# Kernel tuning notes

Measured on AMD Instinct MI355X. Metric: run time of the kernel, lower is better.

Reference implementation:

```python
import jax, jax.numpy as jnp
import numpy as np

B, F, D, V = 8192, 26, 32, 100000
H1, H2 = 128, 128  # cin_size
U1, U2 = 400, 400  # dnn hidden units


def setup_inputs() -> dict:
    key = jax.random.key(0)
    ks = jax.random.split(key, 12)
    s = 0.05  # keep activations/sigmoid in a sane range
    return {
        "dense_inputs": jax.random.normal(ks[0], (B, 13), jnp.float32),
        "sparse_inputs": jax.random.randint(ks[1], (B, F), 0, V, jnp.int32),
        "E": jax.random.normal(ks[2], (F, V, D), jnp.float32) * s,
        "W_cin0": jax.random.normal(ks[3], (F, F, H1), jnp.float32) * s,
        "W_cin1": jax.random.normal(ks[4], (F, H1, H2), jnp.float32) * s,
        "W1": jax.random.normal(ks[5], (F * D, U1), jnp.float32) * s,
        "b1": jnp.zeros((U1,), jnp.float32),
        "W2": jax.random.normal(ks[6], (U1, U2), jnp.float32) * s,
        "b2": jnp.zeros((U2,), jnp.float32),
        "w_lin": jax.random.normal(ks[7], (F, 1), jnp.float32) * s,
        "b_lin": jnp.zeros((1,), jnp.float32),
        "w_out": jax.random.normal(ks[8], (1 + H1 + H2 + U2 + 13, 1), jnp.float32) * s,
        "b_out": jnp.zeros((1,), jnp.float32),
    }


def reference(dense_inputs, sparse_inputs, E, W_cin0, W_cin1, W1, b1, W2, b2,
              w_lin, b_lin, w_out, b_out):
    # Linear part: Dense(1) applied to raw (cast) sparse ids, as in the TF code.
    linear_out = sparse_inputs.astype(jnp.float32) @ w_lin + b_lin  # [B,1]

    # Embedding lookup: per-field tables. embed[b,f,:] = E[f, sparse[b,f], :]
    embed = E[jnp.arange(F)[None, :], sparse_inputs]  # [B,F,D]

    # CIN. The split->matmul->reshape->conv1d chain is exactly:
    #   x_{k+1}[b,h,d] = sum_{i,j} W_k[i,j,h] * X0[b,i,d] * x_k[b,j,d]
    X0 = embed
    x1 = jnp.einsum('bid,bjd,ijh->bhd', X0, X0, W_cin0)   # [B,H1,D]
    x2 = jnp.einsum('bid,bjd,ijh->bhd', X0, x1, W_cin1)   # [B,H2,D]
    cin_out = jnp.concatenate([x1, x2], axis=1).sum(axis=-1)  # [B,H1+H2]

    # DNN on flattened embeddings (dropout rate 0 -> identity at inference).
    v = embed.reshape(B, F * D)
    h = jax.nn.relu(v @ W1 + b1)
    h = jax.nn.relu(h @ W2 + b2)  # [B,U2]

    total = jnp.concatenate([linear_out, cin_out, h, dense_inputs], axis=-1)
    return jax.nn.sigmoid(total @ w_out + b_out)  # [B,1]
```

## Files before the change

### kernel.cpp

```cpp
#include <hip/hip_runtime.h>
#include <hip/hip_bf16.h>
#include <math.h>

typedef __attribute__((ext_vector_type(8))) short bf16x8;
typedef __attribute__((ext_vector_type(4))) float f32x4;

#define B_ 8192
#define F_ 26
#define D_ 32
#define V_ 100000

static const size_t OFF_VB   = 0;
static const size_t OFF_FD0  = 13631488;
static const size_t OFF_H1B  = 13664256;
static const size_t OFF_W1T  = 20217856;
static const size_t OFF_W2T  = 20883456;
static const size_t OFF_K2T  = 21203456;

static __device__ __forceinline__ unsigned short f2b(float f) {
    unsigned int u = __float_as_uint(f);
    return (unsigned short)((u + 0x7FFF + ((u >> 16) & 1)) >> 16);
}
static __device__ __forceinline__ unsigned short f2bt(float f) {
    return (unsigned short)(__float_as_uint(f) >> 16);
}
static __device__ __forceinline__ unsigned int pk2t(float a, float b) {
    return __builtin_amdgcn_perm(__float_as_uint(b), __float_as_uint(a), 0x07060302u);
}
static __device__ __forceinline__ float bf2f(unsigned short u) {
    return __uint_as_float(((unsigned int)u) << 16);
}

static __device__ __forceinline__ void transpose_body(
    const float* __restrict__ src, unsigned short* __restrict__ dst,
    int K, int N, int bx, int by)
{
    __shared__ float tl[32][33];
    const int lx = threadIdx.x & 31, ly = threadIdx.x >> 5;
    const int n0 = bx * 32, k0 = by * 32;
#pragma unroll
    for (int i = 0; i < 4; ++i) {
        int k = k0 + ly + i * 8, n = n0 + lx;
        if (k < K && n < N) tl[ly + i * 8][lx] = src[(size_t)k * N + n];
    }
    __syncthreads();
#pragma unroll
    for (int i = 0; i < 4; ++i) {
        int n = n0 + ly + i * 8, k = k0 + lx;
        if (k < K && n < N) dst[(size_t)n * K + k] = f2b(tl[lx][ly + i * 8]);
    }
}

__global__ __launch_bounds__(256) void k0_all(
    const float* __restrict__ W1, const float* __restrict__ W2,
    const float* __restrict__ W0, const float* __restrict__ Wc1,
    const float* __restrict__ wout,
    unsigned short* __restrict__ W1t, unsigned short* __restrict__ W2t,
    unsigned short* __restrict__ K2T)
{
    __shared__ float Mi[128];
    int bid = blockIdx.x;
    const int t = threadIdx.x;
    if (bid < 338) { transpose_body(W1, W1t, 832, 400, bid % 13, bid / 13); return; }
    bid -= 338;
    if (bid < 169) { transpose_body(W2, W2t, 400, 400, bid % 13, bid / 13); return; }
    bid -= 169;
    const int i = bid;
    if (t < 128) {
        float m = 0.f;
        if (i < F_) {
            const float* row = Wc1 + ((size_t)i * 128 + t) * 128;
            for (int h = 0; h < 128; h += 4) {
                float4 a = *(const float4*)(row + h);
                m = fmaf(a.x, wout[129 + h],     m);
                m = fmaf(a.y, wout[129 + h + 1], m);
                m = fmaf(a.z, wout[129 + h + 2], m);
                m = fmaf(a.w, wout[129 + h + 3], m);
            }
        } else if (i == F_) {
            m = wout[1 + t];
        }
        Mi[t] = m;
    }
    __syncthreads();
    for (int q = t; q < 352; q += 256) {
        float s = 0.f;
        if (q < 351 && i <= F_) {
            int a = 0, base = 0;
            while (base + (F_ - a) <= q) { base += F_ - a; ++a; }
            int b = a + (q - base);
            const float* r0 = W0 + ((size_t)a * F_ + b) * 128;
            const float* r1 = W0 + ((size_t)b * F_ + a) * 128;
            if (a == b) {
                for (int j = 0; j < 128; j += 4) {
                    float4 w = *(const float4*)(r0 + j);
                    s += w.x * Mi[j] + w.y * Mi[j + 1] + w.z * Mi[j + 2] + w.w * Mi[j + 3];
                }
            } else {
                for (int j = 0; j < 128; j += 4) {
                    float4 w  = *(const float4*)(r0 + j);
                    float4 w1 = *(const float4*)(r1 + j);
                    s += (w.x + w1.x) * Mi[j]     + (w.y + w1.y) * Mi[j + 1]
                       + (w.z + w1.z) * Mi[j + 2] + (w.w + w1.w) * Mi[j + 3];
                }
            }
        }
        unsigned short hi = f2b(s);
        float lo = s - bf2f(hi);
        K2T[q * 32 + i] = hi;
        K2T[11264 + q * 32 + i] = f2b(lo);
    }
}

__global__ __launch_bounds__(256) void k1_embed_cin(
    const int*   __restrict__ sparse,
    const float* __restrict__ E,
    const unsigned short* __restrict__ K2T,
    const float* __restrict__ wlin,
    const float* __restrict__ blin,
    const float* __restrict__ wout,
    unsigned short* __restrict__ vb,
    float* __restrict__ fdot0)
{
    __shared__ __align__(16) unsigned short embT[32][40];
    __shared__ unsigned int PQ[352];
    __shared__ int idxs[F_];
    __shared__ float red[4];

    const int b = blockIdx.x, t = threadIdx.x;
    float cind = 0.f;

    if (t < F_) {
        int id = sparse[b * F_ + t];
        idxs[t] = id;
        cind = (float)id * wlin[t] * wout[0];
        int base = F_ * t - (t * (t - 1)) / 2;
        for (int j = t; j < F_; ++j)
            PQ[base + j - t] = (unsigned)t | ((unsigned)j << 16);
    }
    if (t == F_) PQ[351] = 0u;
    if (t >= 32 && t < 64) {
        int d = t - 32;
        embT[d][26] = 0x3F80;
        embT[d][27] = 0; embT[d][28] = 0; embT[d][29] = 0;
        embT[d][30] = 0; embT[d][31] = 0;
    }
    __syncthreads();

    if (t < 208) {
        int f = t >> 3, q = t & 7;
        float4 v4 = *(const float4*)(E + ((size_t)f * V_ + idxs[f]) * D_ + q * 4);
        uint2 uu; uu.x = pk2t(v4.x, v4.y); uu.y = pk2t(v4.z, v4.w);
        *(uint2*)(vb + (size_t)b * 832 + f * 32 + q * 4) = uu;
        embT[q * 4 + 0][f] = f2bt(v4.x);
        embT[q * 4 + 1][f] = f2bt(v4.y);
        embT[q * 4 + 2][f] = f2bt(v4.z);
        embT[q * 4 + 3][f] = f2bt(v4.w);
    }
    __syncthreads();

    const int wave = t >> 6, lane = t & 63;
    const int lr = lane & 15, lg = lane >> 4;
    const int mt = wave & 1;
    const int nb = wave >> 1;
    bf16x8 af = *(const bf16x8*)&embT[mt * 16 + lr][lg * 8];
    const unsigned short* ebase = &embT[mt * 16 + lg * 4][0];
    const unsigned short* Kb = K2T + (size_t)lr * 32 + lg * 8;

#pragma unroll
    for (int s = 0; s < 11; ++s) {
        const int nt = 2 * s + nb;
        bf16x8 bh = *(const bf16x8*)(Kb + (size_t)nt * 512);
        bf16x8 bl = *(const bf16x8*)(Kb + 11264 + (size_t)nt * 512);
        f32x4 h = {};
        h = __builtin_amdgcn_mfma_f32_16x16x32_bf16(af, bl, h, 0, 0, 0);
        h = __builtin_amdgcn_mfma_f32_16x16x32_bf16(af, bh, h, 0, 0, 0);
        unsigned pq = PQ[nt * 16 + lr];
        int oi = (int)(pq & 0xFFFFu), oj = (int)(pq >> 16);
#pragma unroll
        for (int r = 0; r < 4; ++r) {
            float ei = bf2f(ebase[r * 40 + oi]);
            float ej = bf2f(ebase[r * 40 + oj]);
            cind = fmaf(ei * ej, h[r], cind);
        }
    }

#pragma unroll
    for (int off = 1; off <= 32; off <<= 1) cind += __shfl_xor(cind, off, 64);
    if (lane == 0) red[wave] = cind;
    __syncthreads();
    if (t == 0) fdot0[b] = red[0] + red[1] + red[2] + red[3] + blin[0] * wout[0];
}

static __device__ __forceinline__ void gemm_core(
    const unsigned short* __restrict__ A, int lda,
    const unsigned short* __restrict__ Bt, int ldb, int N,
    int m0, int n0, int kbase, int kend,
    unsigned short (*As)[40], unsigned short (*Bs)[40],
    f32x4 (*acc)[2])
{
    const int t = threadIdx.x;
    const int wave = t >> 6, lane = t & 63;
    const int lr = lane & 15, lg = lane >> 4;
    const int wn = wave * 32;
    const int ar = t >> 2, kg = (t & 3) * 8;

    const unsigned short* aptr = A  + (size_t)(m0 + ar) * lda + kbase + kg;
    const unsigned short* bp0  = Bt + (size_t)(n0 + ar) * ldb + kbase + kg;
    const unsigned short* bp1  = Bt + (size_t)(n0 + 64 + ar) * ldb + kbase + kg;
    const bool bn0 = (n0 + ar) < N, bn1 = (n0 + 64 + ar) < N;
    const uint4 z4 = make_uint4(0u, 0u, 0u, 0u);
    const int nkt = (kend - kbase + 31) >> 5;
    uint4 av, bv0, bv1;
    {
        int k = kbase + kg;
        av  = (k < kend)        ? *(const uint4*)aptr : z4;
        bv0 = (bn0 && k < kend) ? *(const uint4*)bp0  : z4;
        bv1 = (bn1 && k < kend) ? *(const uint4*)bp1  : z4;
    }
    for (int kt = 0; kt < nkt; ++kt) {
        *(uint4*)&As[ar][kg]      = av;
        *(uint4*)&Bs[ar][kg]      = bv0;
        *(uint4*)&Bs[64 + ar][kg] = bv1;
        __syncthreads();
        if (kt + 1 < nkt) {
            int kn = kbase + (kt + 1) * 32 + kg;
            av  = (kn < kend)        ? *(const uint4*)(aptr + (kt + 1) * 32) : z4;
            bv0 = (bn0 && kn < kend) ? *(const uint4*)(bp0  + (kt + 1) * 32) : z4;
            bv1 = (bn1 && kn < kend) ? *(const uint4*)(bp1  + (kt + 1) * 32) : z4;
        }
        bf16x8 af[4], bfr[2];
#pragma unroll
        for (int i = 0; i < 4; ++i) af[i]  = *(const bf16x8*)&As[i * 16 + lr][lg * 8];
#pragma unroll
        for (int j = 0; j < 2; ++j) bfr[j] = *(const bf16x8*)&Bs[wn + j * 16 + lr][lg * 8];
#pragma unroll
        for (int i = 0; i < 4; ++i)
#pragma unroll
            for (int j = 0; j < 2; ++j)
                acc[i][j] = __builtin_amdgcn_mfma_f32_16x16x32_bf16(af[i], bfr[j], acc[i][j], 0, 0, 0);
        __syncthreads();
    }
}

__global__ __launch_bounds__(256) void k2_h1(
    const unsigned short* __restrict__ vb, const unsigned short* __restrict__ W1t,
    const float* __restrict__ b1, unsigned short* __restrict__ h1b)
{
    __shared__ __align__(16) unsigned short As[64][40];
    __shared__ __align__(16) unsigned short Bs[128][40];
    const int t = threadIdx.x;
    const int wave = t >> 6, lane = t & 63;
    const int lr = lane & 15, lg = lane >> 4;
    const int m0 = blockIdx.y * 64, n0 = blockIdx.x * 128;
    f32x4 acc[4][2] = {};
    gemm_core(vb, 832, W1t, 832, 400, m0, n0, 0, 832, As, Bs, acc);
#pragma unroll
    for (int i = 0; i < 4; ++i) {
        int mrow = m0 + i * 16 + lg * 4;
#pragma unroll
        for (int j = 0; j < 2; ++j) {
            int col = n0 + wave * 32 + j * 16 + lr;
            if (col >= 400) continue;
            float bb = b1[col];
#pragma unroll
            for (int r = 0; r < 4; ++r)
                h1b[(size_t)(mrow + r) * 400 + col] = f2bt(fmaxf(acc[i][j][r] + bb, 0.f));
        }
    }
}

__global__ __launch_bounds__(256) void k2_h2f(
    const unsigned short* __restrict__ h1b, const unsigned short* __restrict__ W2t,
    const float* __restrict__ b2, const float* __restrict__ wout,
    const float* __restrict__ fdot0, const float* __restrict__ dense,
    const float* __restrict__ bout, float* __restrict__ out)
{
    __shared__ __align__(16) unsigned short As[32][424];
    __shared__ float red[4][32];
    const int t = threadIdx.x;
    const int m0 = blockIdx.x * 32;

    for (int idx = t; idx < 1600; idx += 256) {
        int row = idx / 50, c = idx - row * 50;
        *(uint4*)&As[row][c * 8] = *(const uint4*)(h1b + (size_t)(m0 + row) * 400 + c * 8);
    }
    if (t < 96) {
        int row = t / 3, c = t - row * 3;
        uint4 z = make_uint4(0u, 0u, 0u, 0u);
        *(uint4*)&As[row][400 + c * 8] = z;
    }
    __syncthreads();

    const int wave = t >> 6, lane = t & 63;
    const int lr = lane & 15, lg = lane >> 4;
    float s[2][4] = {};

    for (int nt = wave; nt < 25; nt += 4) {
        f32x4 acc0 = {}, acc1 = {};
        const unsigned short* bp = W2t + (size_t)(nt * 16 + lr) * 400 + lg * 8;
#pragma unroll
        for (int kt = 0; kt < 13; ++kt) {
            const int kk = kt * 32 + lg * 8;
            bf16x8 bw = {};
            if (kk < 400) bw = *(const bf16x8*)(bp + kt * 32);
            bf16x8 a0 = *(const bf16x8*)&As[lr][kk];
            bf16x8 a1 = *(const bf16x8*)&As[16 + lr][kk];
            acc0 = __builtin_amdgcn_mfma_f32_16x16x32_bf16(a0, bw, acc0, 0, 0, 0);
            acc1 = __builtin_amdgcn_mfma_f32_16x16x32_bf16(a1, bw, acc1, 0, 0, 0);
        }
        const int col = nt * 16 + lr;
        const float bb = b2[col], wo = wout[257 + col];
#pragma unroll
        for (int r = 0; r < 4; ++r) {
            s[0][r] = fmaf(fmaxf(acc0[r] + bb, 0.f), wo, s[0][r]);
            s[1][r] = fmaf(fmaxf(acc1[r] + bb, 0.f), wo, s[1][r]);
        }
    }
#pragma unroll
    for (int mt = 0; mt < 2; ++mt)
#pragma unroll
        for (int r = 0; r < 4; ++r) {
            float v = s[mt][r];
            v += __shfl_xor(v, 1, 64);
            v += __shfl_xor(v, 2, 64);
            v += __shfl_xor(v, 4, 64);
            v += __shfl_xor(v, 8, 64);
            if (lr == 0) red[wave][mt * 16 + lg * 4 + r] = v;
        }
    __syncthreads();
    if (t < 32) {
        const int b = m0 + t;
        float tot = red[0][t] + red[1][t] + red[2][t] + red[3][t]
                  + fdot0[b] + bout[0];
#pragma unroll
        for (int q = 0; q < 13; ++q)
            tot = fmaf(dense[(size_t)b * 13 + q], wout[657 + q], tot);
        out[b] = 1.f / (1.f + expf(-tot));
    }
}

extern "C" void kernel_launch(void* const* d_in, const int* in_sizes, int n_in,
                              void* d_out, int out_size, void* d_ws, size_t ws_size,
                              hipStream_t stream) {
    const float* dense  = (const float*)d_in[0];
    const int*   sparse = (const int*)  d_in[1];
    const float* E      = (const float*)d_in[2];
    const float* W0     = (const float*)d_in[3];
    const float* Wc1    = (const float*)d_in[4];
    const float* W1     = (const float*)d_in[5];
    const float* b1     = (const float*)d_in[6];
    const float* W2     = (const float*)d_in[7];
    const float* b2     = (const float*)d_in[8];
    const float* wlin   = (const float*)d_in[9];
    const float* blin   = (const float*)d_in[10];
    const float* wout   = (const float*)d_in[11];
    const float* bout   = (const float*)d_in[12];
    float* out = (float*)d_out;

    char* ws = (char*)d_ws;
    unsigned short* vb    = (unsigned short*)(ws + OFF_VB);
    float*          fdot0 = (float*)(ws + OFF_FD0);
    unsigned short* h1b   = (unsigned short*)(ws + OFF_H1B);
    unsigned short* W1t   = (unsigned short*)(ws + OFF_W1T);
    unsigned short* W2t   = (unsigned short*)(ws + OFF_W2T);
    unsigned short* K2T   = (unsigned short*)(ws + OFF_K2T);

    k0_all<<<338 + 169 + 32, 256, 0, stream>>>(W1, W2, W0, Wc1, wout, W1t, W2t, K2T);
    k1_embed_cin<<<B_, 256, 0, stream>>>(sparse, E, K2T, wlin, blin, wout, vb, fdot0);
    k2_h1<<<dim3(4, 128), 256, 0, stream>>>(vb, W1t, b1, h1b);
    k2_h2f<<<256, 256, 0, stream>>>(h1b, W2t, b2, wout, fdot0, dense, bout, out);
}
```

Measured before the change: 510.9 us.

## Fuse both DNN layers into one kernel keeping hidden activations in LDS

Merges the first-layer GEMM and the second-layer GEMM plus output epilogue into a single 512-thread kernel. Each block holds a 32-row tile of embeddings and keeps the first hidden layer in shared memory, so the h1 round trip through global memory and one launch go away. Weight matrices are transposed and zero-padded to 512 columns so the inner loops need no bounds checks. The trade-off is only 256 blocks for the first GEMM, compared with 512 before, and each block streams the full W1 and W2 from L2 without sharing them through LDS. That lowers parallelism and raises L2 traffic for the weights.

```diff
diff --git a/kernel.cpp b/kernel.cpp
--- a/kernel.cpp
+++ b/kernel.cpp
@@ -12,10 +12,11 @@
 
 static const size_t OFF_VB   = 0;
 static const size_t OFF_FD0  = 13631488;
-static const size_t OFF_H1B  = 13664256;
-static const size_t OFF_W1T  = 20217856;
-static const size_t OFF_W2T  = 20883456;
-static const size_t OFF_K2T  = 21203456;
+static const size_t OFF_W1T  = 13664256;
+static const size_t OFF_W2T  = 14516224;
+static const size_t OFF_K2T  = 15040512;
+static const size_t OFF_B2P  = 15085568;
+static const size_t OFF_WO2P = 15087616;
 
 static __device__ __forceinline__ unsigned short f2b(float f) {
     unsigned int u = __float_as_uint(f);
@@ -31,9 +32,9 @@
     return __uint_as_float(((unsigned int)u) << 16);
 }
 
-static __device__ __forceinline__ void transpose_body(
+static __device__ __forceinline__ void transpose_pad(
     const float* __restrict__ src, unsigned short* __restrict__ dst,
-    int K, int N, int bx, int by)
+    int K, int N, int Kpad, int Npad, int bx, int by)
 {
     __shared__ float tl[32][33];
     const int lx = threadIdx.x & 31, ly = threadIdx.x >> 5;
@@ -41,74 +42,82 @@
 #pragma unroll
     for (int i = 0; i < 4; ++i) {
         int k = k0 + ly + i * 8, n = n0 + lx;
-        if (k < K && n < N) tl[ly + i * 8][lx] = src[(size_t)k * N + n];
+        tl[ly + i * 8][lx] = (k < K && n < N) ? src[(size_t)k * N + n] : 0.f;
     }
     __syncthreads();
 #pragma unroll
     for (int i = 0; i < 4; ++i) {
         int n = n0 + ly + i * 8, k = k0 + lx;
-        if (k < K && n < N) dst[(size_t)n * K + k] = f2b(tl[lx][ly + i * 8]);
+        if (n < Npad && k < Kpad) dst[(size_t)n * Kpad + k] = f2b(tl[lx][ly + i * 8]);
     }
 }
 
 __global__ __launch_bounds__(256) void k0_all(
     const float* __restrict__ W1, const float* __restrict__ W2,
     const float* __restrict__ W0, const float* __restrict__ Wc1,
-    const float* __restrict__ wout,
+    const float* __restrict__ wout, const float* __restrict__ b2,
     unsigned short* __restrict__ W1t, unsigned short* __restrict__ W2t,
-    unsigned short* __restrict__ K2T)
+    unsigned short* __restrict__ K2T,
+    float* __restrict__ b2p, float* __restrict__ wo2p)
 {
     __shared__ float Mi[128];
     int bid = blockIdx.x;
     const int t = threadIdx.x;
-    if (bid < 338) { transpose_body(W1, W1t, 832, 400, bid % 13, bid / 13); return; }
-    bid -= 338;
-    if (bid < 169) { transpose_body(W2, W2t, 400, 400, bid % 13, bid / 13); return; }
-    bid -= 169;
-    const int i = bid;
-    if (t < 128) {
-        float m = 0.f;
-        if (i < F_) {
-            const float* row = Wc1 + ((size_t)i * 128 + t) * 128;
-            for (int h = 0; h < 128; h += 4) {
-                float4 a = *(const float4*)(row + h);
-                m = fmaf(a.x, wout[129 + h],     m);
-                m = fmaf(a.y, wout[129 + h + 1], m);
-                m = fmaf(a.z, wout[129 + h + 2], m);
-                m = fmaf(a.w, wout[129 + h + 3], m);
-            }
-        } else if (i == F_) {
-            m = wout[1 + t];
-        }
-        Mi[t] = m;
-    }
-    __syncthreads();
-    for (int q = t; q < 352; q += 256) {
-        float s = 0.f;
-        if (q < 351 && i <= F_) {
-            int a = 0, base = 0;
-            while (base + (F_ - a) <= q) { base += F_ - a; ++a; }
-            int b = a + (q - base);
-            const float* r0 = W0 + ((size_t)a * F_ + b) * 128;
-            const float* r1 = W0 + ((size_t)b * F_ + a) * 128;
-            if (a == b) {
-                for (int j = 0; j < 128; j += 4) {
-                    float4 w = *(const float4*)(r0 + j);
-                    s += w.x * Mi[j] + w.y * Mi[j + 1] + w.z * Mi[j + 2] + w.w * Mi[j + 3];
+    if (bid < 416) { transpose_pad(W1, W1t, 832, 400, 832, 512, bid % 16, bid / 16); return; }
+    bid -= 416;
+    if (bid < 256) { transpose_pad(W2, W2t, 400, 400, 512, 512, bid % 16, bid / 16); return; }
+    bid -= 256;
+    if (bid < 32) {
+        const int i = bid;
+        if (t < 128) {
+            float m = 0.f;
+            if (i < F_) {
+                const float* row = Wc1 + ((size_t)i * 128 + t) * 128;
+                for (int h = 0; h < 128; h += 4) {
+                    float4 a = *(const float4*)(row + h);
+                    m = fmaf(a.x, wout[129 + h],     m);
+                    m = fmaf(a.y, wout[129 + h + 1], m);
+                    m = fmaf(a.z, wout[129 + h + 2], m);
+                    m = fmaf(a.w, wout[129 + h + 3], m);
                 }
-            } else {
-                for (int j = 0; j < 128; j += 4) {
-                    float4 w  = *(const float4*)(r0 + j);
-                    float4 w1 = *(const float4*)(r1 + j);
-                    s += (w.x + w1.x) * Mi[j]     + (w.y + w1.y) * Mi[j + 1]
-                       + (w.z + w1.z) * Mi[j + 2] + (w.w + w1.w) * Mi[j + 3];
+            } else if (i == F_) {
+                m = wout[1 + t];
+            }
+            Mi[t] = m;
+        }
+        __syncthreads();
+        for (int q = t; q < 352; q += 256) {
+            float s = 0.f;
+            if (q < 351 && i <= F_) {
+                int a = 0, base = 0;
+                while (base + (F_ - a) <= q) { base += F_ - a; ++a; }
+                int b = a + (q - base);
+                const float* r0 = W0 + ((size_t)a * F_ + b) * 128;
+                const float* r1 = W0 + ((size_t)b * F_ + a) * 128;
+                if (a == b) {
+                    for (int j = 0; j < 128; j += 4) {
+                        float4 w = *(const float4*)(r0 + j);
+                        s += w.x * Mi[j] + w.y * Mi[j + 1] + w.z * Mi[j + 2] + w.w * Mi[j + 3];
+                    }
+                } else {
+                    for (int j = 0; j < 128; j += 4) {
+                        float4 w  = *(const float4*)(r0 + j);
+                        float4 w1 = *(const float4*)(r1 + j);
+                        s += (w.x + w1.x) * Mi[j]     + (w.y + w1.y) * Mi[j + 1]
+                           + (w.z + w1.z) * Mi[j + 2] + (w.w + w1.w) * Mi[j + 3];
+                    }
                 }
             }
-        }
-        unsigned short hi = f2b(s);
-        float lo = s - bf2f(hi);
-        K2T[q * 32 + i] = hi;
-        K2T[11264 + q * 32 + i] = f2b(lo);
+            unsigned short hi = f2b(s);
+            float lo = s - bf2f(hi);
+            K2T[q * 32 + i] = hi;
+            K2T[11264 + q * 32 + i] = f2b(lo);
+        }
+        return;
+    }
+    for (int c = t; c < 512; c += 256) {
+        b2p[c]  = (c < 400) ? b2[c] : 0.f;
+        wo2p[c] = (c < 400) ? wout[257 + c] : 0.f;
     }
 }
 
@@ -192,147 +201,135 @@
     if (t == 0) fdot0[b] = red[0] + red[1] + red[2] + red[3] + blin[0] * wout[0];
 }
 
-static __device__ __forceinline__ void gemm_core(
-    const unsigned short* __restrict__ A, int lda,
-    const unsigned short* __restrict__ Bt, int ldb, int N,
-    int m0, int n0, int kbase, int kend,
-    unsigned short (*As)[40], unsigned short (*Bs)[40],
-    f32x4 (*acc)[2])
+__global__ __launch_bounds__(512) void k23_mlp(
+    const unsigned short* __restrict__ vb,
+    const unsigned short* __restrict__ W1t,
+    const unsigned short* __restrict__ W2t,
+    const float* __restrict__ b1,
+    const float* __restrict__ b2p,
+    const float* __restrict__ wo2p,
+    const float* __restrict__ fdot0,
+    const float* __restrict__ dense,
+    const float* __restrict__ wout,
+    const float* __restrict__ bout,
+    float* __restrict__ out)
 {
+    __shared__ __align__(16) unsigned short As1[32][840];
+    __shared__ __align__(16) unsigned short h1s[32][520];
+    __shared__ float red[8][32];
+
     const int t = threadIdx.x;
+    const int m0 = blockIdx.x * 32;
+
+    {
+        const int row = t >> 4, c0 = t & 15;
+        const unsigned short* src = vb + (size_t)(m0 + row) * 832;
+#pragma unroll
+        for (int j = 0; j < 7; ++j) {
+            int c = c0 + j * 16;
+            if (c < 104) *(uint4*)&As1[row][c * 8] = *(const uint4*)(src + c * 8);
+        }
+    }
+    __syncthreads();
+
     const int wave = t >> 6, lane = t & 63;
     const int lr = lane & 15, lg = lane >> 4;
-    const int wn = wave * 32;
-    const int ar = t >> 2, kg = (t & 3) * 8;
-
-    const unsigned short* aptr = A  + (size_t)(m0 + ar) * lda + kbase + kg;
-    const unsigned short* bp0  = Bt + (size_t)(n0 + ar) * ldb + kbase + kg;
-    const unsigned short* bp1  = Bt + (size_t)(n0 + 64 + ar) * ldb + kbase + kg;
-    const bool bn0 = (n0 + ar) < N, bn1 = (n0 + 64 + ar) < N;
-    const uint4 z4 = make_uint4(0u, 0u, 0u, 0u);
-    const int nkt = (kend - kbase + 31) >> 5;
-    uint4 av, bv0, bv1;
+
     {
-        int k = kbase + kg;
-        av  = (k < kend)        ? *(const uint4*)aptr : z4;
-        bv0 = (bn0 && k < kend) ? *(const uint4*)bp0  : z4;
-        bv1 = (bn1 && k < kend) ? *(const uint4*)bp1  : z4;
-    }
-    for (int kt = 0; kt < nkt; ++kt) {
-        *(uint4*)&As[ar][kg]      = av;
-        *(uint4*)&Bs[ar][kg]      = bv0;
-        *(uint4*)&Bs[64 + ar][kg] = bv1;
-        __syncthreads();
-        if (kt + 1 < nkt) {
-            int kn = kbase + (kt + 1) * 32 + kg;
-            av  = (kn < kend)        ? *(const uint4*)(aptr + (kt + 1) * 32) : z4;
-            bv0 = (bn0 && kn < kend) ? *(const uint4*)(bp0  + (kt + 1) * 32) : z4;
-            bv1 = (bn1 && kn < kend) ? *(const uint4*)(bp1  + (kt + 1) * 32) : z4;
-        }
-        bf16x8 af[4], bfr[2];
-#pragma unroll
-        for (int i = 0; i < 4; ++i) af[i]  = *(const bf16x8*)&As[i * 16 + lr][lg * 8];
-#pragma unroll
-        for (int j = 0; j < 2; ++j) bfr[j] = *(const bf16x8*)&Bs[wn + j * 16 + lr][lg * 8];
-#pragma unroll
-        for (int i = 0; i < 4; ++i)
-#pragma unroll
-            for (int j = 0; j < 2; ++j)
-                acc[i][j] = __builtin_amdgcn_mfma_f32_16x16x32_bf16(af[i], bfr[j], acc[i][j], 0, 0, 0);
-        __syncthreads();
-    }
-}
-
-__global__ __launch_bounds__(256) void k2_h1(
-    const unsigned short* __restrict__ vb, const unsigned short* __restrict__ W1t,
-    const float* __restrict__ b1, unsigned short* __restrict__ h1b)
-{
-    __shared__ __align__(16) unsigned short As[64][40];
-    __shared__ __align__(16) unsigned short Bs[128][40];
-    const int t = threadIdx.x;
-    const int wave = t >> 6, lane = t & 63;
-    const int lr = lane & 15, lg = lane >> 4;
-    const int m0 = blockIdx.y * 64, n0 = blockIdx.x * 128;
-    f32x4 acc[4][2] = {};
-    gemm_core(vb, 832, W1t, 832, 400, m0, n0, 0, 832, As, Bs, acc);
-#pragma unroll
-    for (int i = 0; i < 4; ++i) {
-        int mrow = m0 + i * 16 + lg * 4;
-#pragma unroll
-        for (int j = 0; j < 2; ++j) {
-            int col = n0 + wave * 32 + j * 16 + lr;
-            if (col >= 400) continue;
-            float bb = b1[col];
-#pragma unroll
-            for (int r = 0; r < 4; ++r)
-                h1b[(size_t)(mrow + r) * 400 + col] = f2bt(fmaxf(acc[i][j][r] + bb, 0.f));
-        }
-    }
-}
-
-__global__ __launch_bounds__(256) void k2_h2f(
-    const unsigned short* __restrict__ h1b, const unsigned short* __restrict__ W2t,
-    const float* __restrict__ b2, const float* __restrict__ wout,
-    const float* __restrict__ fdot0, const float* __restrict__ dense,
-    const float* __restrict__ bout, float* __restrict__ out)
-{
-    __shared__ __align__(16) unsigned short As[32][424];
-    __shared__ float red[4][32];
-    const int t = threadIdx.x;
-    const int m0 = blockIdx.x * 32;
-
-    for (int idx = t; idx < 1600; idx += 256) {
-        int row = idx / 50, c = idx - row * 50;
-        *(uint4*)&As[row][c * 8] = *(const uint4*)(h1b + (size_t)(m0 + row) * 400 + c * 8);
-    }
-    if (t < 96) {
-        int row = t / 3, c = t - row * 3;
-        uint4 z = make_uint4(0u, 0u, 0u, 0u);
-        *(uint4*)&As[row][400 + c * 8] = z;
-    }
-    __syncthreads();
-
-    const int wave = t >> 6, lane = t & 63;
-    const int lr = lane & 15, lg = lane >> 4;
-    float s[2][4] = {};
-
-    for (int nt = wave; nt < 25; nt += 4) {
-        f32x4 acc0 = {}, acc1 = {};
-        const unsigned short* bp = W2t + (size_t)(nt * 16 + lr) * 400 + lg * 8;
-#pragma unroll
-        for (int kt = 0; kt < 13; ++kt) {
+        f32x4 acc[4][2] = {};
+        const unsigned short* bp0 = W1t + (size_t)((wave +  0) * 16 + lr) * 832 + lg * 8;
+        const unsigned short* bp1 = W1t + (size_t)((wave +  8) * 16 + lr) * 832 + lg * 8;
+        const unsigned short* bp2 = W1t + (size_t)((wave + 16) * 16 + lr) * 832 + lg * 8;
+        const unsigned short* bp3 = W1t + (size_t)((wave + 24) * 16 + lr) * 832 + lg * 8;
+#pragma unroll 2
+        for (int kt = 0; kt < 26; ++kt) {
             const int kk = kt * 32 + lg * 8;
-            bf16x8 bw = {};
-            if (kk < 400) bw = *(const bf16x8*)(bp + kt * 32);
-            bf16x8 a0 = *(const bf16x8*)&As[lr][kk];
-            bf16x8 a1 = *(const bf16x8*)&As[16 + lr][kk];
-            acc0 = __builtin_amdgcn_mfma_f32_16x16x32_bf16(a0, bw, acc0, 0, 0, 0);
-            acc1 = __builtin_amdgcn_mfma_f32_16x16x32_bf16(a1, bw, acc1, 0, 0, 0);
-        }
-        const int col = nt * 16 + lr;
-        const float bb = b2[col], wo = wout[257 + col];
+            bf16x8 a0 = *(const bf16x8*)&As1[lr][kk];
+            bf16x8 a1 = *(const bf16x8*)&As1[16 + lr][kk];
+            bf16x8 b0 = *(const bf16x8*)(bp0 + kt * 32);
+            bf16x8 b1w = *(const bf16x8*)(bp1 + kt * 32);
+            bf16x8 b2w = *(const bf16x8*)(bp2 + kt * 32);
+            bf16x8 b3w = *(const bf16x8*)(bp3 + kt * 32);
+            acc[0][0] = __builtin_amdgcn_mfma_f32_16x16x32_bf16(a0, b0,  acc[0][0], 0, 0, 0);
+            acc[0][1] = __builtin_amdgcn_mfma_f32_16x16x32_bf16(a1, b0,  acc[0][1], 0, 0, 0);
+            acc[1][0] = __builtin_amdgcn_mfma_f32_16x16x32_bf16(a0, b1w, acc[1][0], 0, 0, 0);
+            acc[1][1] = __builtin_amdgcn_mfma_f32_16x16x32_bf16(a1, b1w, acc[1][1], 0, 0, 0);
+            acc[2][0] = __builtin_amdgcn_mfma_f32_16x16x32_bf16(a0, b2w, acc[2][0], 0, 0, 0);
+            acc[2][1] = __builtin_amdgcn_mfma_f32_16x16x32_bf16(a1, b2w, acc[2][1], 0, 0, 0);
+            acc[3][0] = __builtin_amdgcn_mfma_f32_16x16x32_bf16(a0, b3w, acc[3][0], 0, 0, 0);
+            acc[3][1] = __builtin_amdgcn_mfma_f32_16x16x32_bf16(a1, b3w, acc[3][1], 0, 0, 0);
+        }
+#pragma unroll
+        for (int q = 0; q < 4; ++q) {
+            const int col = (wave + 8 * q) * 16 + lr;
+            const bool vld = col < 400;
+            const float bb = vld ? b1[col] : 0.f;
+#pragma unroll
+            for (int r = 0; r < 4; ++r) {
+                float v0 = fmaxf(acc[q][0][r] + bb, 0.f);
+                float v1 = fmaxf(acc[q][1][r] + bb, 0.f);
+                h1s[lg * 4 + r][col]      = vld ? f2bt(v0) : (unsigned short)0;
+                h1s[16 + lg * 4 + r][col] = vld ? f2bt(v1) : (unsigned short)0;
+            }
+        }
+    }
+    __syncthreads();
+
+    {
+        f32x4 acc[4][2] = {};
+        const unsigned short* bp0 = W2t + (size_t)((wave +  0) * 16 + lr) * 512 + lg * 8;
+        const unsigned short* bp1 = W2t + (size_t)((wave +  8) * 16 + lr) * 512 + lg * 8;
+        const unsigned short* bp2 = W2t + (size_t)((wave + 16) * 16 + lr) * 512 + lg * 8;
+        const unsigned short* bp3 = W2t + (size_t)((wave + 24) * 16 + lr) * 512 + lg * 8;
+#pragma unroll 2
+        for (int kt = 0; kt < 16; ++kt) {
+            const int kk = kt * 32 + lg * 8;
+            bf16x8 a0 = *(const bf16x8*)&h1s[lr][kk];
+            bf16x8 a1 = *(const bf16x8*)&h1s[16 + lr][kk];
+            bf16x8 b0 = *(const bf16x8*)(bp0 + kt * 32);
+            bf16x8 b1w = *(const bf16x8*)(bp1 + kt * 32);
+            bf16x8 b2w = *(const bf16x8*)(bp2 + kt * 32);
+            bf16x8 b3w = *(const bf16x8*)(bp3 + kt * 32);
+            acc[0][0] = __builtin_amdgcn_mfma_f32_16x16x32_bf16(a0, b0,  acc[0][0], 0, 0, 0);
+            acc[0][1] = __builtin_amdgcn_mfma_f32_16x16x32_bf16(a1, b0,  acc[0][1], 0, 0, 0);
+            acc[1][0] = __builtin_amdgcn_mfma_f32_16x16x32_bf16(a0, b1w, acc[1][0], 0, 0, 0);
+            acc[1][1] = __builtin_amdgcn_mfma_f32_16x16x32_bf16(a1, b1w, acc[1][1], 0, 0, 0);
+            acc[2][0] = __builtin_amdgcn_mfma_f32_16x16x32_bf16(a0, b2w, acc[2][0], 0, 0, 0);
+            acc[2][1] = __builtin_amdgcn_mfma_f32_16x16x32_bf16(a1, b2w, acc[2][1], 0, 0, 0);
+            acc[3][0] = __builtin_amdgcn_mfma_f32_16x16x32_bf16(a0, b3w, acc[3][0], 0, 0, 0);
+            acc[3][1] = __builtin_amdgcn_mfma_f32_16x16x32_bf16(a1, b3w, acc[3][1], 0, 0, 0);
+        }
+        float s0[4] = {0.f, 0.f, 0.f, 0.f}, s1[4] = {0.f, 0.f, 0.f, 0.f};
+#pragma unroll
+        for (int q = 0; q < 4; ++q) {
+            const int col = (wave + 8 * q) * 16 + lr;
+            const float bb = b2p[col], wo = wo2p[col];
+#pragma unroll
+            for (int r = 0; r < 4; ++r) {
+                s0[r] = fmaf(fmaxf(acc[q][0][r] + bb, 0.f), wo, s0[r]);
+                s1[r] = fmaf(fmaxf(acc[q][1][r] + bb, 0.f), wo, s1[r]);
+            }
+        }
 #pragma unroll
         for (int r = 0; r < 4; ++r) {
-            s[0][r] = fmaf(fmaxf(acc0[r] + bb, 0.f), wo, s[0][r]);
-            s[1][r] = fmaf(fmaxf(acc1[r] + bb, 0.f), wo, s[1][r]);
-        }
-    }
-#pragma unroll
-    for (int mt = 0; mt < 2; ++mt)
-#pragma unroll
-        for (int r = 0; r < 4; ++r) {
-            float v = s[mt][r];
-            v += __shfl_xor(v, 1, 64);
-            v += __shfl_xor(v, 2, 64);
-            v += __shfl_xor(v, 4, 64);
-            v += __shfl_xor(v, 8, 64);
-            if (lr == 0) red[wave][mt * 16 + lg * 4 + r] = v;
-        }
-    __syncthreads();
+            float v0 = s0[r], v1 = s1[r];
+            v0 += __shfl_xor(v0, 1, 64); v1 += __shfl_xor(v1, 1, 64);
+            v0 += __shfl_xor(v0, 2, 64); v1 += __shfl_xor(v1, 2, 64);
+            v0 += __shfl_xor(v0, 4, 64); v1 += __shfl_xor(v1, 4, 64);
+            v0 += __shfl_xor(v0, 8, 64); v1 += __shfl_xor(v1, 8, 64);
+            if (lr == 0) {
+                red[wave][lg * 4 + r] = v0;
+                red[wave][16 + lg * 4 + r] = v1;
+            }
+        }
+    }
+    __syncthreads();
+
     if (t < 32) {
         const int b = m0 + t;
-        float tot = red[0][t] + red[1][t] + red[2][t] + red[3][t]
-                  + fdot0[b] + bout[0];
+        float tot = fdot0[b] + bout[0];
+#pragma unroll
+        for (int w = 0; w < 8; ++w) tot += red[w][t];
 #pragma unroll
         for (int q = 0; q < 13; ++q)
             tot = fmaf(dense[(size_t)b * 13 + q], wout[657 + q], tot);
@@ -361,13 +358,15 @@
     char* ws = (char*)d_ws;
     unsigned short* vb    = (unsigned short*)(ws + OFF_VB);
     float*          fdot0 = (float*)(ws + OFF_FD0);
-    unsigned short* h1b   = (unsigned short*)(ws + OFF_H1B);
     unsigned short* W1t   = (unsigned short*)(ws + OFF_W1T);
     unsigned short* W2t   = (unsigned short*)(ws + OFF_W2T);
     unsigned short* K2T   = (unsigned short*)(ws + OFF_K2T);
-
-    k0_all<<<338 + 169 + 32, 256, 0, stream>>>(W1, W2, W0, Wc1, wout, W1t, W2t, K2T);
+    float*          b2p   = (float*)(ws + OFF_B2P);
+    float*          wo2p  = (float*)(ws + OFF_WO2P);
+
+    k0_all<<<416 + 256 + 32 + 1, 256, 0, stream>>>(W1, W2, W0, Wc1, wout, b2,
+                                                   W1t, W2t, K2T, b2p, wo2p);
     k1_embed_cin<<<B_, 256, 0, stream>>>(sparse, E, K2T, wlin, blin, wout, vb, fdot0);
-    k2_h1<<<dim3(4, 128), 256, 0, stream>>>(vb, W1t, b1, h1b);
-    k2_h2f<<<256, 256, 0, stream>>>(h1b, W2t, b2, wout, fdot0, dense, bout, out);
-}
+    k23_mlp<<<256, 512, 0, stream>>>(vb, W1t, W2t, b1, b2p, wo2p,
+                                     fdot0, dense, wout, bout, out);
+}
```

After: 506.5 us. No clear change (-0.9%).
